# Optimization experiments

Measured on AMD Instinct MI355X. Metric: run time of the kernel, lower is better.

Reference implementation:

```python
import jax, jax.numpy as jnp
import numpy as np

C_IN, HIDDEN, C_OUT, N_NODE = 200, 128, 2, 200
BATCH = 512

def setup_inputs() -> dict:
    key = jax.random.key(0)
    k1, k2, k3, k4 = jax.random.split(key, 4)
    x = jax.random.normal(k1, (BATCH, N_NODE, C_IN), dtype=jnp.float32)
    adj = jax.random.randint(k2, (BATCH, N_NODE, N_NODE), 0, 2, dtype=jnp.int32)
    # GINConv MLPs (single Linear each); stored as [in, out]
    W1 = jax.random.normal(k3, (C_IN, HIDDEN), dtype=jnp.float32) / np.sqrt(C_IN)
    b1 = jnp.zeros((HIDDEN,), dtype=jnp.float32)
    W2 = jax.random.normal(k4, (HIDDEN, C_OUT), dtype=jnp.float32) / np.sqrt(HIDDEN)
    b2 = jnp.zeros((C_OUT,), dtype=jnp.float32)
    eps1 = jnp.zeros((), dtype=jnp.float32)  # train_eps=True, init 0
    eps2 = jnp.zeros((), dtype=jnp.float32)
    return {"x": x, "adj": adj, "W1": W1, "b1": b1, "W2": W2, "b2": b2, "eps1": eps1, "eps2": eps2}

def _gin_aggregate(adjf, h):
    # edge (b,i,j) sends h[b,i] to node j: agg[b,j] = sum_i adj[b,i,j]*h[b,i]
    return jnp.einsum('bij,bif->bjf', adjf, h)

def reference(x, adj, W1, b1, W2, b2, eps1, eps2):
    adjf = adj.astype(x.dtype)  # binary 0/1 adjacency [B,N,N]
    # GIN layer 1: nn((1+eps)*x + sum_neighbors(x)), then ReLU
    agg1 = _gin_aggregate(adjf, x)
    h = jax.nn.relu(((1.0 + eps1) * x + agg1) @ W1 + b1)
    # GIN layer 2
    agg2 = _gin_aggregate(adjf, h)
    out = ((1.0 + eps2) * h + agg2) @ W2 + b2  # [B,N,2]
    return out.mean(axis=-2)  # [B,2]
```

## Files before the change

### kernel.cpp

```cpp
#include <hip/hip_runtime.h>

#define BATCH 512
#define NNODE 200
#define CIN   200
#define HID   128
#define IPY   232
#define KCH   7

typedef __attribute__((ext_vector_type(4))) float  f32x4;
typedef __attribute__((ext_vector_type(4))) int    i32x4;
typedef __attribute__((ext_vector_type(8))) short  sh8;
typedef __attribute__((ext_vector_type(4))) short  sh4;
typedef __attribute__((ext_vector_type(8))) __bf16 bf16x8;

__device__ __forceinline__ short f2bf(float x) {
  union { float f; unsigned u; } v; v.f = x;
  unsigned r = v.u + 0x7FFFu + ((v.u >> 16) & 1u);
  return (short)(r >> 16);
}
__device__ __forceinline__ f32x4 mfma16(sh8 a, sh8 b, f32x4 c) {
  return __builtin_amdgcn_mfma_f32_16x16x32_bf16(
      __builtin_bit_cast(bf16x8, a), __builtin_bit_cast(bf16x8, b), c, 0, 0, 0);
}
__device__ __forceinline__ f32x4 mfma16i(sh8 a, i32x4 b, f32x4 c) {
  return __builtin_amdgcn_mfma_f32_16x16x32_bf16(
      __builtin_bit_cast(bf16x8, a), __builtin_bit_cast(bf16x8, b), c, 0, 0, 0);
}
__device__ __forceinline__ i32x4 expand8(unsigned byte_) {
  i32x4 w;
#pragma unroll
  for (int h = 0; h < 4; ++h) {
    unsigned p = byte_ >> (2 * h);
    unsigned d = ((p & 1u) ? 0x3F80u : 0u) | ((p & 2u) ? 0x3F800000u : 0u);
    w[h] = (int)d;
  }
  return w;
}

__global__ __launch_bounds__(256) void k_prep(const float* __restrict__ W1,
                                              short* __restrict__ W1T) {
  const int idx = blockIdx.x * 256 + threadIdx.x;
  const int f = idx / IPY, c = idx - f * IPY;
  W1T[idx] = (c < CIN) ? f2bf(W1[(size_t)c * HID + f]) : (short)0;
}

__global__ __launch_bounds__(1024) void k_gin(const float* __restrict__ x,
                                              const int* __restrict__ adj,
                                              const short* __restrict__ W1Tg,
                                              const float* __restrict__ b1,
                                              const float* __restrict__ W2,
                                              const float* __restrict__ b2,
                                              const float* __restrict__ eps1p,
                                              const float* __restrict__ eps2p,
                                              float* __restrict__ out) {
  __shared__ short    ls_w1t[HID * IPY];
  __shared__ short    ls_y  [HID * IPY];
  __shared__ unsigned ls_bits[224 * 8];
  __shared__ float    ls_deg[224];
  __shared__ float    ls_part[13][2];

  const int b    = blockIdx.x;
  const int tid  = threadIdx.x;
  const int wave = tid >> 6, lane = tid & 63;
  const int lq   = lane >> 4, lm = lane & 15;
  const float e1 = eps1p[0], e2 = eps2p[0];
  const int* adjb = adj + (size_t)b * NNODE * NNODE;

  if (wave < 4) {
    const int j  = wave * 64 + lane;
    const int jc = min(j, NNODE - 1);
    unsigned w[8] = {0, 0, 0, 0, 0, 0, 0, 0};
#pragma unroll
    for (int wd = 0; wd < 7; ++wd) {
      const int cnt = (wd < 6) ? 32 : 8;
      unsigned a = 0;
#pragma unroll
      for (int t = 0; t < 32; ++t)
        if (t < cnt) a |= (unsigned)(adjb[(wd * 32 + t) * NNODE + jc] & 1) << t;
      w[wd] = a;
    }
    if (j < 224) {
      const bool jv = (j < NNODE);
#pragma unroll
      for (int wd = 0; wd < 8; ++wd) ls_bits[j * 8 + wd] = jv ? w[wd] : 0u;
    }
  } else if (wave < 8) {
    const int v = wave - 4;
#pragma unroll 2
    for (int r = 0; r < 50; ++r) {
      const int i = v * 50 + r;
      const int* rp = adjb + (size_t)i * NNODE;
      int s = rp[lane] + rp[64 + lane] + rp[128 + lane] + ((lane < 8) ? rp[192 + lane] : 0);
#pragma unroll
      for (int d = 1; d < 64; d <<= 1) s += __shfl_xor(s, d);
      if (lane == 0) ls_deg[i] = (float)s;
    }
  } else {
#pragma unroll
    for (int it = 0; it < 8; ++it) {
      const int c = (wave - 8) + it * 8;
      if (c < 58)
        *(sh8*)&ls_w1t[c * 512 + lane * 8] = *(const sh8*)(W1Tg + c * 512 + lane * 8);
    }
    const int q = tid - 512;
    if (q < 384) {
      const int f = q / 3, p = q - f * 3;
      sh8 z = {0, 0, 0, 0, 0, 0, 0, 0};
      *(sh8*)&ls_y[f * IPY + 200 + p * 8] = z;
    } else if (q < 408) {
      ls_deg[200 + q - 384] = 0.f;
    }
  }
  __syncthreads();

  if (wave < 13) {
    const int mt  = wave;
    const int row = min(mt * 16 + lm, NNODE - 1);
    const float* xr = x + (size_t)b * NNODE * CIN + (size_t)row * CIN;
    sh8 af[KCH];
#pragma unroll
    for (int k = 0; k < KCH; ++k) {
      const int c0 = k * 32 + lq * 8;
      f32x4 p0 = {0.f, 0.f, 0.f, 0.f}, p1 = {0.f, 0.f, 0.f, 0.f};
      if (c0 < CIN) { p0 = *(const f32x4*)(xr + c0); p1 = *(const f32x4*)(xr + c0 + 4); }
      sh8 a;
#pragma unroll
      for (int jj = 0; jj < 4; ++jj) { a[jj] = f2bf(p0[jj]); a[4 + jj] = f2bf(p1[jj]); }
      af[k] = a;
    }
#pragma unroll 2
    for (int ft = 0; ft < 8; ++ft) {
      const int fb = ft * 16;
      const short* wr = &ls_w1t[(fb + lm) * IPY];
      f32x4 acc = {0.f, 0.f, 0.f, 0.f};
#pragma unroll
      for (int k = 0; k < KCH; ++k)
        acc = mfma16(af[k], *(const sh8*)(wr + k * 32 + lq * 8), acc);
      sh4 st;
#pragma unroll
      for (int r = 0; r < 4; ++r) st[r] = f2bf(acc[r]);
      if (mt * 16 + lq * 4 < NNODE)
        *(sh4*)&ls_y[(fb + lm) * IPY + mt * 16 + lq * 4] = st;
    }
  }
  __syncthreads();

  if (wave < 13) {
    const int jt = wave;
    const int j  = jt * 16 + lm;
    const bool jok = (j < NNODE);
    const unsigned cd0 = (unsigned)(unsigned short)f2bf(1.f + e1);
    const unsigned cd1 = (unsigned)(unsigned short)f2bf(2.f + e1);
    unsigned bwa[8];
    *(i32x4*)&bwa[0] = *(const i32x4*)&ls_bits[j * 8];
    *(i32x4*)&bwa[4] = *(const i32x4*)&ls_bits[j * 8 + 4];
    i32x4 bfr[KCH];
#pragma unroll
    for (int k = 0; k < KCH; ++k) {
      const unsigned byte_ = (bwa[k] >> (lq * 8)) & 0xFFu;
      i32x4 w = expand8(byte_);
      const int d = j - (k * 32 + lq * 8);
      if (d >= 0 && d < 8) {
        const unsigned val = ((byte_ >> d) & 1u) ? cd1 : cd0;
        const int h2 = d >> 1, sh = (d & 1) * 16;
        w[h2] = (int)(((unsigned)w[h2] & ~(0xFFFFu << sh)) | (val << sh));
      }
      bfr[k] = w;
    }
    float ga = 0.f, gb = 0.f;
#pragma unroll 2
    for (int ft = 0; ft < 8; ++ft) {
      const int fb = ft * 16;
      const short* yr = &ls_y[(fb + lm) * IPY];
      f32x4 acc = {0.f, 0.f, 0.f, 0.f};
#pragma unroll
      for (int k = 0; k < KCH; ++k)
        acc = mfma16i(*(const sh8*)(yr + k * 32 + lq * 8), bfr[k], acc);
      const f32x4 b1v = *(const f32x4*)(b1 + fb + lq * 4);
      const f32x4 w2a = *(const f32x4*)(W2 + (fb + lq * 4) * 2);
      const f32x4 w2b = *(const f32x4*)(W2 + (fb + lq * 4) * 2 + 4);
#pragma unroll
      for (int r = 0; r < 4; ++r) {
        const float h = fmaxf(acc[r] + b1v[r], 0.f);
        const float wc0 = (r == 0) ? w2a[0] : (r == 1) ? w2a[2] : (r == 2) ? w2b[0] : w2b[2];
        const float wc1 = (r == 0) ? w2a[1] : (r == 1) ? w2a[3] : (r == 2) ? w2b[1] : w2b[3];
        ga += h * wc0;
        gb += h * wc1;
      }
    }
    ga += __shfl_xor(ga, 16); ga += __shfl_xor(ga, 32);
    gb += __shfl_xor(gb, 16); gb += __shfl_xor(gb, 32);
    const float wj = 1.f + e2 + ls_deg[min(j, NNODE - 1)];
    float t0 = jok ? wj * ga : 0.f;
    float t1 = jok ? wj * gb : 0.f;
#pragma unroll
    for (int d = 1; d < 16; d <<= 1) { t0 += __shfl_xor(t0, d); t1 += __shfl_xor(t1, d); }
    if (lane == 0) { ls_part[jt][0] = t0; ls_part[jt][1] = t1; }
  }
  __syncthreads();

  if (tid < 2) {
    float s = 0.f;
#pragma unroll
    for (int q = 0; q < 13; ++q) s += ls_part[q][tid];
    out[b * 2 + tid] = b2[tid] + s * (1.f / NNODE);
  }
}

extern "C" void kernel_launch(void* const* d_in, const int* in_sizes, int n_in,
                              void* d_out, int out_size, void* d_ws, size_t ws_size,
                              hipStream_t stream) {
  const float* x    = (const float*)d_in[0];
  const int*   adj  = (const int*)d_in[1];
  const float* W1   = (const float*)d_in[2];
  const float* b1   = (const float*)d_in[3];
  const float* W2   = (const float*)d_in[4];
  const float* b2   = (const float*)d_in[5];
  const float* eps1 = (const float*)d_in[6];
  const float* eps2 = (const float*)d_in[7];
  float* out = (float*)d_out;

  short* W1T = (short*)d_ws;

  k_prep<<<116, 256, 0, stream>>>(W1, W1T);
  k_gin <<<BATCH, 1024, 0, stream>>>(x, adj, W1T, b1, W2, b2, eps1, eps2, out);
}
```

Before: 240.6 us.

## Split adjacency bit-packing across 12 waves, derive degrees via ballot, prefetch x early

Adjacency bit-packing is now spread over 12 waves, each covering a row group and column chunk, instead of 4 waves doing all rows serially. Row degrees come from ballot/popcount of the loaded bits rather than a separate pass that re-reads adjacency rows, and partial counts are summed in the GEMM phase by the idle waves. The x rows are loaded into registers before the first barrier so their global latency overlaps the adjacency loads. This costs more registers (the 14 prefetched float4 values per thread) and moves the W1 staging onto fewer waves.

```diff
diff --git a/kernel.cpp b/kernel.cpp
--- a/kernel.cpp
+++ b/kernel.cpp
@@ -55,7 +55,8 @@
                                               float* __restrict__ out) {
   __shared__ short    ls_w1t[HID * IPY];
   __shared__ short    ls_y  [HID * IPY];
-  __shared__ unsigned ls_bits[224 * 8];
+  __shared__ unsigned ls_bits[KCH * 224];
+  __shared__ int      ls_degp[4 * 224];
   __shared__ float    ls_deg[224];
   __shared__ float    ls_part[13][2];
 
@@ -66,66 +67,88 @@
   const float e1 = eps1p[0], e2 = eps2p[0];
   const int* adjb = adj + (size_t)b * NNODE * NNODE;
 
-  if (wave < 4) {
-    const int j  = wave * 64 + lane;
-    const int jc = min(j, NNODE - 1);
-    unsigned w[8] = {0, 0, 0, 0, 0, 0, 0, 0};
-#pragma unroll
-    for (int wd = 0; wd < 7; ++wd) {
-      const int cnt = (wd < 6) ? 32 : 8;
-      unsigned a = 0;
-#pragma unroll
-      for (int t = 0; t < 32; ++t)
-        if (t < cnt) a |= (unsigned)(adjb[(wd * 32 + t) * NNODE + jc] & 1) << t;
-      w[wd] = a;
-    }
-    if (j < 224) {
-      const bool jv = (j < NNODE);
-#pragma unroll
-      for (int wd = 0; wd < 8; ++wd) ls_bits[j * 8 + wd] = jv ? w[wd] : 0u;
-    }
-  } else if (wave < 8) {
-    const int v = wave - 4;
-#pragma unroll 2
-    for (int r = 0; r < 50; ++r) {
-      const int i = v * 50 + r;
-      const int* rp = adjb + (size_t)i * NNODE;
-      int s = rp[lane] + rp[64 + lane] + rp[128 + lane] + ((lane < 8) ? rp[192 + lane] : 0);
-#pragma unroll
-      for (int d = 1; d < 64; d <<= 1) s += __shfl_xor(s, d);
-      if (lane == 0) ls_deg[i] = (float)s;
-    }
-  } else {
-#pragma unroll
-    for (int it = 0; it < 8; ++it) {
-      const int c = (wave - 8) + it * 8;
-      if (c < 58)
-        *(sh8*)&ls_w1t[c * 512 + lane * 8] = *(const sh8*)(W1Tg + c * 512 + lane * 8);
-    }
-    const int q = tid - 512;
-    if (q < 384) {
-      const int f = q / 3, p = q - f * 3;
-      sh8 z = {0, 0, 0, 0, 0, 0, 0, 0};
-      *(sh8*)&ls_y[f * IPY + 200 + p * 8] = z;
-    } else if (q < 408) {
-      ls_deg[200 + q - 384] = 0.f;
-    }
-  }
-  __syncthreads();
-
+  f32x4 px0[KCH], px1[KCH];
   if (wave < 13) {
-    const int mt  = wave;
-    const int row = min(mt * 16 + lm, NNODE - 1);
+    const int row = min(wave * 16 + lm, NNODE - 1);
     const float* xr = x + (size_t)b * NNODE * CIN + (size_t)row * CIN;
-    sh8 af[KCH];
 #pragma unroll
     for (int k = 0; k < KCH; ++k) {
       const int c0 = k * 32 + lq * 8;
-      f32x4 p0 = {0.f, 0.f, 0.f, 0.f}, p1 = {0.f, 0.f, 0.f, 0.f};
-      if (c0 < CIN) { p0 = *(const f32x4*)(xr + c0); p1 = *(const f32x4*)(xr + c0 + 4); }
+      f32x4 z = {0.f, 0.f, 0.f, 0.f};
+      px0[k] = z; px1[k] = z;
+      if (c0 < CIN) { px0[k] = *(const f32x4*)(xr + c0); px1[k] = *(const f32x4*)(xr + c0 + 4); }
+    }
+  }
+
+  if (wave < 12) {
+    const int g = wave >> 2, c = wave & 3;
+    const int j = c * 64 + lane;
+    const int jc = min(j, NNODE - 1);
+    const unsigned jv = (j < NNODE) ? 1u : 0u;
+    const int base = g * 64;
+    unsigned wa0 = 0, wa1 = 0, wa2 = 0;
+#pragma unroll
+    for (int t = 0; t < 32; ++t) {
+      const int r = base + t;
+      const unsigned v = (unsigned)adjb[r * NNODE + jc] & 1u;
+      wa0 |= v << t;
+      const unsigned long long m = __ballot(v & jv);
+      if (lane == 0) ls_degp[c * 224 + r] = __popcll(m);
+    }
+#pragma unroll
+    for (int t = 0; t < 32; ++t) {
+      const int r = base + 32 + t;
+      const unsigned v = (unsigned)adjb[r * NNODE + jc] & 1u;
+      wa1 |= v << t;
+      const unsigned long long m = __ballot(v & jv);
+      if (lane == 0) ls_degp[c * 224 + r] = __popcll(m);
+    }
+    if (g == 2) {
+#pragma unroll
+      for (int t = 0; t < 8; ++t) {
+        const int r = 192 + t;
+        const unsigned v = (unsigned)adjb[r * NNODE + jc] & 1u;
+        wa2 |= v << t;
+        const unsigned long long m = __ballot(v & jv);
+        if (lane == 0) ls_degp[c * 224 + r] = __popcll(m);
+      }
+    }
+    if (j < 224) {
+      ls_bits[(g * 2 + 0) * 224 + j] = jv ? wa0 : 0u;
+      ls_bits[(g * 2 + 1) * 224 + j] = jv ? wa1 : 0u;
+      if (g == 2) ls_bits[6 * 224 + j] = jv ? wa2 : 0u;
+    }
+  } else {
+    const int wq = wave - 12;
+    const int c0 = (wq == 0) ? 0 : 10 + (wq - 1) * 16;
+    const int nc = (wq == 0) ? 10 : 16;
+    for (int it = 0; it < nc; ++it) {
+      const int ch = c0 + it;
+      *(sh8*)&ls_w1t[ch * 512 + lane * 8] = *(const sh8*)(W1Tg + ch * 512 + lane * 8);
+    }
+    if (wave >= 13) {
+      const int q = tid - 832;
+#pragma unroll
+      for (int it = 0; it < 3; ++it) {
+        const int idx = q + it * 192;
+        if (idx < 512) {
+          const int f = idx >> 2, p = idx & 3;
+          sh8 z = {0, 0, 0, 0, 0, 0, 0, 0};
+          *(sh8*)&ls_y[f * IPY + 200 + p * 8] = z;
+        }
+      }
+    }
+  }
+  __syncthreads();
+
+  if (wave < 13) {
+    const int mt = wave;
+    sh8 af[KCH];
+#pragma unroll
+    for (int k = 0; k < KCH; ++k) {
       sh8 a;
 #pragma unroll
-      for (int jj = 0; jj < 4; ++jj) { a[jj] = f2bf(p0[jj]); a[4 + jj] = f2bf(p1[jj]); }
+      for (int jj = 0; jj < 4; ++jj) { a[jj] = f2bf(px0[k][jj]); a[4 + jj] = f2bf(px1[k][jj]); }
       af[k] = a;
     }
 #pragma unroll 2
@@ -141,6 +164,14 @@
       for (int r = 0; r < 4; ++r) st[r] = f2bf(acc[r]);
       if (mt * 16 + lq * 4 < NNODE)
         *(sh4*)&ls_y[(fb + lm) * IPY + mt * 16 + lq * 4] = st;
+    }
+  } else {
+    const int q = tid - 832;
+    for (int r = q; r < 224; r += 192) {
+      int s = 0;
+      if (r < NNODE)
+        s = ls_degp[r] + ls_degp[224 + r] + ls_degp[448 + r] + ls_degp[672 + r];
+      ls_deg[r] = (float)s;
     }
   }
   __syncthreads();
@@ -151,9 +182,9 @@
     const bool jok = (j < NNODE);
     const unsigned cd0 = (unsigned)(unsigned short)f2bf(1.f + e1);
     const unsigned cd1 = (unsigned)(unsigned short)f2bf(2.f + e1);
-    unsigned bwa[8];
-    *(i32x4*)&bwa[0] = *(const i32x4*)&ls_bits[j * 8];
-    *(i32x4*)&bwa[4] = *(const i32x4*)&ls_bits[j * 8 + 4];
+    unsigned bwa[KCH];
+#pragma unroll
+    for (int k = 0; k < KCH; ++k) bwa[k] = ls_bits[k * 224 + j];
     i32x4 bfr[KCH];
 #pragma unroll
     for (int k = 0; k < KCH; ++k) {
```

Result: slower. 265.0 us (+10.2%).

## Coalesce adjacency loads, fuse degree via ballot, overlap x loads with staging

Applied to the files above, without the earlier changes.

Adjacency bit-packing moves to three waves that read whole rows coalesced, 8 rows at a time, and compute node degrees with ballot/popcount in the same pass. This removes the separate strided column gather and the second full adjacency read for degrees. The x loads and bf16 conversion for the first GEMM now happen in the 13 compute waves before the first barrier, overlapping with the adjacency work, and W1T staging is spread across those waves. The bit array layout changes to word-major, and launch bounds gain an occupancy hint. More registers are held across the barrier, which may pressure occupancy.

```diff
diff --git a/kernel.cpp b/kernel.cpp
--- a/kernel.cpp
+++ b/kernel.cpp
@@ -44,90 +44,99 @@
   W1T[idx] = (c < CIN) ? f2bf(W1[(size_t)c * HID + f]) : (short)0;
 }
 
-__global__ __launch_bounds__(1024) void k_gin(const float* __restrict__ x,
-                                              const int* __restrict__ adj,
-                                              const short* __restrict__ W1Tg,
-                                              const float* __restrict__ b1,
-                                              const float* __restrict__ W2,
-                                              const float* __restrict__ b2,
-                                              const float* __restrict__ eps1p,
-                                              const float* __restrict__ eps2p,
-                                              float* __restrict__ out) {
-  __shared__ short    ls_w1t[HID * IPY];
-  __shared__ short    ls_y  [HID * IPY];
-  __shared__ unsigned ls_bits[224 * 8];
-  __shared__ float    ls_deg[224];
-  __shared__ float    ls_part[13][2];
+__global__ __launch_bounds__(1024, 4) void k_gin(const float* __restrict__ x,
+                                                 const int* __restrict__ adj,
+                                                 const short* __restrict__ W1Tg,
+                                                 const float* __restrict__ b1,
+                                                 const float* __restrict__ W2,
+                                                 const float* __restrict__ b2,
+                                                 const float* __restrict__ eps1p,
+                                                 const float* __restrict__ eps2p,
+                                                 float* __restrict__ out) {
+  __shared__ __align__(16) short    ls_w1t[HID * IPY];
+  __shared__ __align__(16) short    ls_y  [HID * IPY];
+  __shared__ __align__(16) unsigned ls_bits[KCH * 224];
+  __shared__ __align__(16) float    ls_deg[224];
+  __shared__               float    ls_part[13][2];
 
   const int b    = blockIdx.x;
   const int tid  = threadIdx.x;
   const int wave = tid >> 6, lane = tid & 63;
   const int lq   = lane >> 4, lm = lane & 15;
-  const float e1 = eps1p[0], e2 = eps2p[0];
   const int* adjb = adj + (size_t)b * NNODE * NNODE;
 
-  if (wave < 4) {
-    const int j  = wave * 64 + lane;
-    const int jc = min(j, NNODE - 1);
-    unsigned w[8] = {0, 0, 0, 0, 0, 0, 0, 0};
-#pragma unroll
-    for (int wd = 0; wd < 7; ++wd) {
-      const int cnt = (wd < 6) ? 32 : 8;
-      unsigned a = 0;
-#pragma unroll
-      for (int t = 0; t < 32; ++t)
-        if (t < cnt) a |= (unsigned)(adjb[(wd * 32 + t) * NNODE + jc] & 1) << t;
-      w[wd] = a;
-    }
-    if (j < 224) {
-      const bool jv = (j < NNODE);
-#pragma unroll
-      for (int wd = 0; wd < 8; ++wd) ls_bits[j * 8 + wd] = jv ? w[wd] : 0u;
-    }
-  } else if (wave < 8) {
-    const int v = wave - 4;
-#pragma unroll 2
-    for (int r = 0; r < 50; ++r) {
-      const int i = v * 50 + r;
-      const int* rp = adjb + (size_t)i * NNODE;
-      int s = rp[lane] + rp[64 + lane] + rp[128 + lane] + ((lane < 8) ? rp[192 + lane] : 0);
-#pragma unroll
-      for (int d = 1; d < 64; d <<= 1) s += __shfl_xor(s, d);
-      if (lane == 0) ls_deg[i] = (float)s;
+  sh8 af[KCH];
+
+  if (wave >= 13) {
+    const int iw  = wave - 13;
+    const int wd0 = iw * 2, wd1 = (iw == 2) ? 7 : iw * 2 + 2;
+    const int jc3 = min(192 + lane, NNODE - 1);
+    for (int wd = wd0; wd < wd1; ++wd) {
+      const int tmax = (wd == 6) ? 8 : 32;
+      unsigned w0 = 0, w1 = 0, w2 = 0, w3 = 0;
+      for (int t8 = 0; t8 < tmax; t8 += 8) {
+        int v0[8], v1[8], v2[8], v3[8];
+#pragma unroll
+        for (int rr = 0; rr < 8; ++rr) {
+          const int* rp = adjb + (wd * 32 + t8 + rr) * NNODE;
+          v0[rr] = rp[lane]; v1[rr] = rp[64 + lane];
+          v2[rr] = rp[128 + lane]; v3[rr] = rp[jc3];
+        }
+#pragma unroll
+        for (int rr = 0; rr < 8; ++rr) {
+          const int t = t8 + rr;
+          const unsigned b0 = (unsigned)v0[rr] & 1u;
+          const unsigned b1_ = (unsigned)v1[rr] & 1u;
+          const unsigned b2_ = (unsigned)v2[rr] & 1u;
+          const unsigned b3_ = (lane < 8) ? ((unsigned)v3[rr] & 1u) : 0u;
+          w0 |= b0 << t; w1 |= b1_ << t; w2 |= b2_ << t; w3 |= b3_ << t;
+          const int dg = __popcll(__ballot(b0 != 0u)) + __popcll(__ballot(b1_ != 0u))
+                       + __popcll(__ballot(b2_ != 0u)) + __popcll(__ballot(b3_ != 0u));
+          if (lane == 0) ls_deg[wd * 32 + t] = (float)dg;
+        }
+      }
+      unsigned* bp = &ls_bits[wd * 224];
+      bp[lane] = w0; bp[64 + lane] = w1; bp[128 + lane] = w2;
+      if (lane < 32) bp[192 + lane] = w3;
     }
   } else {
-#pragma unroll
-    for (int it = 0; it < 8; ++it) {
-      const int c = (wave - 8) + it * 8;
-      if (c < 58)
-        *(sh8*)&ls_w1t[c * 512 + lane * 8] = *(const sh8*)(W1Tg + c * 512 + lane * 8);
-    }
-    const int q = tid - 512;
-    if (q < 384) {
-      const int f = q / 3, p = q - f * 3;
+    sh8 sc[5];
+    int chs[5];
+#pragma unroll
+    for (int it = 0; it < 5; ++it) {
+      chs[it] = wave + it * 13;
+      if (chs[it] < 58) sc[it] = ((const sh8*)W1Tg)[chs[it] * 64 + lane];
+    }
+    f32x4 px0[KCH], px1[KCH];
+    const int row = min(wave * 16 + lm, NNODE - 1);
+    const float* xr = x + (size_t)b * NNODE * CIN + (size_t)row * CIN;
+#pragma unroll
+    for (int k = 0; k < KCH; ++k) {
+      const int c0 = k * 32 + lq * 8;
+      f32x4 z = {0.f, 0.f, 0.f, 0.f};
+      px0[k] = z; px1[k] = z;
+      if (c0 < CIN) { px0[k] = *(const f32x4*)(xr + c0); px1[k] = *(const f32x4*)(xr + c0 + 4); }
+    }
+#pragma unroll
+    for (int it = 0; it < 5; ++it)
+      if (chs[it] < 58) ((sh8*)ls_w1t)[chs[it] * 64 + lane] = sc[it];
+    if (tid < 384) {
+      const int f = tid / 3, p = tid - f * 3;
       sh8 z = {0, 0, 0, 0, 0, 0, 0, 0};
       *(sh8*)&ls_y[f * IPY + 200 + p * 8] = z;
-    } else if (q < 408) {
-      ls_deg[200 + q - 384] = 0.f;
+    }
+#pragma unroll
+    for (int k = 0; k < KCH; ++k) {
+      sh8 a;
+#pragma unroll
+      for (int jj = 0; jj < 4; ++jj) { a[jj] = f2bf(px0[k][jj]); a[4 + jj] = f2bf(px1[k][jj]); }
+      af[k] = a;
     }
   }
   __syncthreads();
 
   if (wave < 13) {
-    const int mt  = wave;
-    const int row = min(mt * 16 + lm, NNODE - 1);
-    const float* xr = x + (size_t)b * NNODE * CIN + (size_t)row * CIN;
-    sh8 af[KCH];
-#pragma unroll
-    for (int k = 0; k < KCH; ++k) {
-      const int c0 = k * 32 + lq * 8;
-      f32x4 p0 = {0.f, 0.f, 0.f, 0.f}, p1 = {0.f, 0.f, 0.f, 0.f};
-      if (c0 < CIN) { p0 = *(const f32x4*)(xr + c0); p1 = *(const f32x4*)(xr + c0 + 4); }
-      sh8 a;
-#pragma unroll
-      for (int jj = 0; jj < 4; ++jj) { a[jj] = f2bf(p0[jj]); a[4 + jj] = f2bf(p1[jj]); }
-      af[k] = a;
-    }
+    const int mt = wave;
 #pragma unroll 2
     for (int ft = 0; ft < 8; ++ft) {
       const int fb = ft * 16;
@@ -146,14 +155,15 @@
   __syncthreads();
 
   if (wave < 13) {
+    const float e1 = eps1p[0], e2 = eps2p[0];
     const int jt = wave;
     const int j  = jt * 16 + lm;
     const bool jok = (j < NNODE);
     const unsigned cd0 = (unsigned)(unsigned short)f2bf(1.f + e1);
     const unsigned cd1 = (unsigned)(unsigned short)f2bf(2.f + e1);
-    unsigned bwa[8];
-    *(i32x4*)&bwa[0] = *(const i32x4*)&ls_bits[j * 8];
-    *(i32x4*)&bwa[4] = *(const i32x4*)&ls_bits[j * 8 + 4];
+    unsigned bwa[KCH];
+#pragma unroll
+    for (int k = 0; k < KCH; ++k) bwa[k] = ls_bits[k * 224 + j];
     i32x4 bfr[KCH];
 #pragma unroll
     for (int k = 0; k < KCH; ++k) {
```

Measured after the change: 211.0 us. 12.3% less time.
